# Kernel tuning notes

Hardware: AMD Instinct MI355X
Metric: run time of the kernel (lower is better)

Reference implementation:

```python
import jax, jax.numpy as jnp
import numpy as np

N_NODES = 100000
N_EDGES = 3200000
DIM = 64
N_LAYERS = 3


def setup_inputs() -> dict:
    key = jax.random.key(0)
    ks = jax.random.split(key, 8)
    x = jax.random.normal(ks[0], (N_NODES, DIM), dtype=jnp.float32)
    a = jax.random.uniform(ks[1], (N_EDGES,), dtype=jnp.float32)
    # weights stored as [in_dim, out_dim] so layer op is h @ W + b
    W1s = jax.random.normal(ks[2], (N_LAYERS, DIM, DIM), dtype=jnp.float32) * (1.0 / np.sqrt(DIM))
    b1s = jnp.zeros((N_LAYERS, DIM), dtype=jnp.float32)
    W2s = jax.random.normal(ks[3], (N_LAYERS, DIM, DIM), dtype=jnp.float32) * (1.0 / np.sqrt(DIM))
    b2s = jnp.zeros((N_LAYERS, DIM), dtype=jnp.float32)
    src = jax.random.randint(ks[4], (N_EDGES,), 0, N_NODES, dtype=jnp.int32)
    dst = jax.random.randint(ks[5], (N_EDGES,), 0, N_NODES, dtype=jnp.int32)
    return {"x": x, "a": a, "W1s": W1s, "b1s": b1s, "W2s": W2s, "b2s": b2s,
            "src": src, "dst": dst}


def reference(x, a, W1s, b1s, W2s, b2s, src, dst):
    """KGAT forward (eval mode, dropouts=0, normalize=False, full-graph blocks).

    Per layer: h_n[v] = sum_{e:(u->v)} a_e * h[u]
               h <- LeakyReLU((h + h_n) @ W1 + b1) + LeakyReLU((h * h_n) @ W2 + b2)
    Output: concat([x, h_1, h_2, h_3], axis=1) -> [N, 4*DIM]
    """
    n = x.shape[0]
    h = x
    embs = [x]
    for l in range(N_LAYERS):
        msg = h[src] * a[:, None]                      # [E, d] gather + edge scale
        h_n = jax.ops.segment_sum(msg, dst, num_segments=n)  # [N, d] scatter-add
        h = (jax.nn.leaky_relu((h + h_n) @ W1s[l] + b1s[l], 0.01)
             + jax.nn.leaky_relu((h * h_n) @ W2s[l] + b2s[l], 0.01))
        embs.append(h)
    return jnp.concatenate(embs, axis=1)
```

## Files before the change

kernel.cpp:

```cpp
#include <hip/hip_runtime.h>
#include <hip/hip_bf16.h>

#define N_NODES 100000
#define N_EDGES 3200000
#define DIM 64
#define OUT_COLS 256
#define BUCKET_SHIFT 8
#define NBUCK ((N_NODES + 255) / 256)
#define TILE 4096
#define NTILEBLK ((N_EDGES + TILE - 1) / TILE)
#define NODE_TILES ((N_NODES + 63) / 64)
#define WFRAG_PER_LAYER (2 * 2 * 4 * 64 * 8)

typedef __attribute__((ext_vector_type(8))) short short8;
typedef __attribute__((ext_vector_type(4))) float f32x4;

__device__ __forceinline__ unsigned short f2bf(float f) {
    __hip_bfloat16 b = __float2bfloat16(f);
    unsigned short u;
    __builtin_memcpy(&u, &b, 2);
    return u;
}
__device__ __forceinline__ unsigned int pkbf(float a, float b) {
    return (unsigned int)f2bf(a) | ((unsigned int)f2bf(b) << 16);
}
__device__ __forceinline__ float bflo(unsigned int p) { return __uint_as_float(p << 16); }
__device__ __forceinline__ float bfhi(unsigned int p) { return __uint_as_float(p & 0xFFFF0000u); }

__global__ void init_kernel(const float* __restrict__ x,
                            float* __restrict__ h,
                            unsigned short* __restrict__ h_bf,
                            float* __restrict__ out) {
    int i = blockIdx.x * blockDim.x + threadIdx.x;
    const int total = N_NODES * DIM / 4;
    if (i < total) {
        float4 v = ((const float4*)x)[i];
        ((float4*)h)[i] = v;
        int elem = i * 4;
        int node = elem >> 6;
        int c    = elem & 63;
        *(float4*)&out[node * OUT_COLS + c] = v;
        unsigned int lo = pkbf(v.x, v.y);
        unsigned int hi = pkbf(v.z, v.w);
        *(uint2*)&h_bf[elem] = make_uint2(lo, hi);
    }
}

__global__ __launch_bounds__(256) void wprep_kernel(const float* __restrict__ W1s,
                                                    const float* __restrict__ W2s,
                                                    unsigned short* __restrict__ wfrag) {
    int idx = blockIdx.x * 256 + threadIdx.x;
    if (idx >= 3 * WFRAG_PER_LAYER) return;
    int j     = idx & 7;
    int lane  = (idx >> 3) & 63;
    int ct    = (idx >> 9) & 3;
    int kt    = (idx >> 11) & 1;
    int mat   = (idx >> 12) & 1;
    int layer = idx >> 13;
    int k   = kt * 32 + (lane >> 4) * 8 + j;
    int col = ct * 16 + (lane & 15);
    const float* W = (mat ? W2s : W1s) + (size_t)layer * DIM * DIM;
    wfrag[idx] = f2bf(W[k * DIM + col]);
}

__global__ __launch_bounds__(256) void bucket_hist_kernel(const int* __restrict__ dst,
                                                          int* __restrict__ bucket_count) {
    __shared__ int lc[NBUCK];
    for (int b = threadIdx.x; b < NBUCK; b += 256) lc[b] = 0;
    __syncthreads();
    const int base = blockIdx.x * TILE;
#pragma unroll
    for (int k = 0; k < TILE / 256; ++k) {
        int e = base + k * 256 + threadIdx.x;
        if (e < N_EDGES) atomicAdd(&lc[((unsigned)dst[e]) >> BUCKET_SHIFT], 1);
    }
    __syncthreads();
    for (int b = threadIdx.x; b < NBUCK; b += 256) {
        int c = lc[b];
        if (c) atomicAdd(&bucket_count[b], c);
    }
}

__global__ __launch_bounds__(512) void bucket_scan_kernel(const int* __restrict__ bucket_count,
                                                          int* __restrict__ bucket_base,
                                                          int* __restrict__ bucket_cursor,
                                                          int* __restrict__ offsets) {
    __shared__ int s[512];
    const int t = threadIdx.x;
    int v = (t < NBUCK) ? bucket_count[t] : 0;
    s[t] = v;
    __syncthreads();
    for (int off = 1; off < 512; off <<= 1) {
        int u = (t >= off) ? s[t - off] : 0;
        __syncthreads();
        s[t] += u;
        __syncthreads();
    }
    if (t < NBUCK) { int b = s[t] - v; bucket_base[t] = b; bucket_cursor[t] = b; }
    if (t == 0) offsets[N_NODES] = N_EDGES;
}

__global__ __launch_bounds__(256) void binA_kernel(const int* __restrict__ src,
                                                   const int* __restrict__ dst,
                                                   const float* __restrict__ a,
                                                   int* __restrict__ bucket_cursor,
                                                   int2* __restrict__ temp) {
    __shared__ int lcount[NBUCK];
    __shared__ int lscan[512];
    __shared__ int lgbase[NBUCK];
    __shared__ int2 stage[TILE];
    __shared__ unsigned short sbuck[TILE];

    const int t = threadIdx.x;
    const int base = blockIdx.x * TILE;

    for (int b = t; b < NBUCK; b += 256) lcount[b] = 0;
    __syncthreads();

    int dv[TILE / 256], rk[TILE / 256];
#pragma unroll
    for (int k = 0; k < TILE / 256; ++k) {
        int e = base + k * 256 + t;
        dv[k] = 0; rk[k] = 0;
        if (e < N_EDGES) {
            int d = dst[e];
            dv[k] = d;
            rk[k] = atomicAdd(&lcount[((unsigned)d) >> BUCKET_SHIFT], 1);
        }
    }
    __syncthreads();

    lscan[t]       = (t < NBUCK) ? lcount[t] : 0;
    lscan[t + 256] = (t + 256 < NBUCK) ? lcount[t + 256] : 0;
    __syncthreads();
    for (int off = 1; off < 512; off <<= 1) {
        int u0 = (t >= off) ? lscan[t - off] : 0;
        int u1 = ((t + 256) >= off) ? lscan[t + 256 - off] : 0;
        __syncthreads();
        lscan[t] += u0;
        lscan[t + 256] += u1;
        __syncthreads();
    }
    for (int b = t; b < NBUCK; b += 256) {
        int c = lcount[b];
        int excl = lscan[b] - c;
        int g = 0;
        if (c) g = atomicAdd(&bucket_cursor[b], c);
        lgbase[b] = g - excl;
    }
    __syncthreads();

#pragma unroll
    for (int k = 0; k < TILE / 256; ++k) {
        int e = base + k * 256 + t;
        if (e < N_EDGES) {
            int d = dv[k];
            int b = ((unsigned)d) >> BUCKET_SHIFT;
            int slot = (lscan[b] - lcount[b]) + rk[k];
            stage[slot] = make_int2(src[e] | ((d & 255) << 24), __float_as_int(a[e]));
            sbuck[slot] = (unsigned short)b;
        }
    }
    __syncthreads();

    const int cntT = min(TILE, N_EDGES - base);
    for (int i = t; i < cntT; i += 256) {
        temp[lgbase[sbuck[i]] + i] = stage[i];
    }
}

__global__ __launch_bounds__(256) void binB_kernel(const int2* __restrict__ temp,
                                                   const int* __restrict__ bucket_base,
                                                   const int* __restrict__ bucket_count,
                                                   int* __restrict__ offsets,
                                                   int2* __restrict__ edges) {
    const int b = blockIdx.x;
    const int node0 = b << BUCKET_SHIFT;
    const int nodes = min(256, N_NODES - node0);
    const int beg = bucket_base[b];
    const int cnt = bucket_count[b];
    const int t = threadIdx.x;

    __shared__ int ncount[256];
    __shared__ int ssc[256];
    __shared__ int ncur[256];
    ncount[t] = 0;
    __syncthreads();
    for (int i = t; i < cnt; i += 256) {
        unsigned w0 = (unsigned)temp[beg + i].x;
        atomicAdd(&ncount[w0 >> 24], 1);
    }
    __syncthreads();
    int v = ncount[t];
    ssc[t] = v;
    __syncthreads();
    for (int off = 1; off < 256; off <<= 1) {
        int u = (t >= off) ? ssc[t - off] : 0;
        __syncthreads();
        ssc[t] += u;
        __syncthreads();
    }
    int excl = ssc[t] - v;
    if (t < nodes) offsets[node0 + t] = beg + excl;
    ncur[t] = beg + excl;
    __syncthreads();
    for (int i = t; i < cnt; i += 256) {
        int2 r = temp[beg + i];
        int loc = ((unsigned)r.x) >> 24;
        int pos = atomicAdd(&ncur[loc], 1);
        edges[pos] = make_int2(r.x & 0xFFFFFF, r.y);
    }
}

__global__ __launch_bounds__(256) void gather_kernel(
        const unsigned short* __restrict__ h_bf,
        const int2* __restrict__ edges,
        const int* __restrict__ offsets,
        float* __restrict__ hn) {
    const int lane   = threadIdx.x & 63;
    const int half   = lane >> 5;
    const int sub    = lane & 31;
    const int waveid = (blockIdx.x * blockDim.x + threadIdx.x) >> 6;
    const int node   = waveid * 2 + half;
    if (node >= N_NODES) return;

    const int beg = offsets[node];
    const int end = offsets[node + 1];
    const int col2 = sub * 2;

    float al0 = 0.f, al1 = 0.f, al2 = 0.f, al3 = 0.f;
    float ah0 = 0.f, ah1 = 0.f, ah2 = 0.f, ah3 = 0.f;
    int i = beg;
    for (; i + 4 <= end; i += 4) {
        int2 e0 = edges[i + 0];
        int2 e1 = edges[i + 1];
        int2 e2 = edges[i + 2];
        int2 e3 = edges[i + 3];
        unsigned int p0 = *(const unsigned int*)&h_bf[(size_t)e0.x * DIM + col2];
        unsigned int p1 = *(const unsigned int*)&h_bf[(size_t)e1.x * DIM + col2];
        unsigned int p2 = *(const unsigned int*)&h_bf[(size_t)e2.x * DIM + col2];
        unsigned int p3 = *(const unsigned int*)&h_bf[(size_t)e3.x * DIM + col2];
        float w0 = __int_as_float(e0.y);
        float w1 = __int_as_float(e1.y);
        float w2 = __int_as_float(e2.y);
        float w3 = __int_as_float(e3.y);
        al0 = fmaf(w0, bflo(p0), al0);  ah0 = fmaf(w0, bfhi(p0), ah0);
        al1 = fmaf(w1, bflo(p1), al1);  ah1 = fmaf(w1, bfhi(p1), ah1);
        al2 = fmaf(w2, bflo(p2), al2);  ah2 = fmaf(w2, bfhi(p2), ah2);
        al3 = fmaf(w3, bflo(p3), al3);  ah3 = fmaf(w3, bfhi(p3), ah3);
    }
    for (; i < end; ++i) {
        int2 e = edges[i];
        unsigned int p = *(const unsigned int*)&h_bf[(size_t)e.x * DIM + col2];
        float w = __int_as_float(e.y);
        al0 = fmaf(w, bflo(p), al0);
        ah0 = fmaf(w, bfhi(p), ah0);
    }
    float lo = (al0 + al1) + (al2 + al3);
    float hi = (ah0 + ah1) + (ah2 + ah3);
    *(float2*)&hn[(size_t)node * DIM + col2] = make_float2(lo, hi);
}

__global__ __launch_bounds__(256) void update_kernel(
        float* __restrict__ h,
        unsigned short* __restrict__ h_bf,
        const float* __restrict__ hn,
        const unsigned short* __restrict__ wfrag,
        const float* __restrict__ b1,
        const float* __restrict__ b2,
        float* __restrict__ out,
        int out_col_base) {
    __shared__ unsigned short t1s[64 * 64];
    __shared__ unsigned short t2s[64 * 64];

    const int t    = threadIdx.x;
    const int lane = t & 63;
    const int wid  = t >> 6;
    const int node0 = blockIdx.x * 64;

    short8 w1f[2][4], w2f[2][4];
#pragma unroll
    for (int kt = 0; kt < 2; ++kt)
#pragma unroll
        for (int ct = 0; ct < 4; ++ct) {
            w1f[kt][ct] = *(const short8*)(wfrag + (((0 * 2 + kt) * 4 + ct) * 64 + lane) * 8);
            w2f[kt][ct] = *(const short8*)(wfrag + (((1 * 2 + kt) * 4 + ct) * 64 + lane) * 8);
        }
    float bb1[4], bb2[4];
#pragma unroll
    for (int ct = 0; ct < 4; ++ct) {
        bb1[ct] = b1[ct * 16 + (lane & 15)];
        bb2[ct] = b2[ct * 16 + (lane & 15)];
    }

    {
        const int row = t >> 2;
        const int kc  = (t & 3) * 16;
        const int node = node0 + row;
        float tv1[16], tv2[16];
        if (node < N_NODES) {
            const float4* hp  = (const float4*)&h [(size_t)node * DIM + kc];
            const float4* hnp = (const float4*)&hn[(size_t)node * DIM + kc];
#pragma unroll
            for (int i = 0; i < 4; ++i) {
                float4 a = hp[i];
                float4 b = hnp[i];
                tv1[i * 4 + 0] = a.x + b.x;  tv2[i * 4 + 0] = a.x * b.x;
                tv1[i * 4 + 1] = a.y + b.y;  tv2[i * 4 + 1] = a.y * b.y;
                tv1[i * 4 + 2] = a.z + b.z;  tv2[i * 4 + 2] = a.z * b.z;
                tv1[i * 4 + 3] = a.w + b.w;  tv2[i * 4 + 3] = a.w * b.w;
            }
        } else {
#pragma unroll
            for (int i = 0; i < 16; ++i) { tv1[i] = 0.f; tv2[i] = 0.f; }
        }
        const int sw = (row & 7) << 4;
        const int base = row * 128 + (t & 3) * 32;
        uint4 q;
        q.x = pkbf(tv1[0], tv1[1]);  q.y = pkbf(tv1[2], tv1[3]);
        q.z = pkbf(tv1[4], tv1[5]);  q.w = pkbf(tv1[6], tv1[7]);
        *(uint4*)((char*)t1s + ((base) ^ sw)) = q;
        q.x = pkbf(tv1[8], tv1[9]);  q.y = pkbf(tv1[10], tv1[11]);
        q.z = pkbf(tv1[12], tv1[13]); q.w = pkbf(tv1[14], tv1[15]);
        *(uint4*)((char*)t1s + ((base + 16) ^ sw)) = q;
        q.x = pkbf(tv2[0], tv2[1]);  q.y = pkbf(tv2[2], tv2[3]);
        q.z = pkbf(tv2[4], tv2[5]);  q.w = pkbf(tv2[6], tv2[7]);
        *(uint4*)((char*)t2s + ((base) ^ sw)) = q;
        q.x = pkbf(tv2[8], tv2[9]);  q.y = pkbf(tv2[10], tv2[11]);
        q.z = pkbf(tv2[12], tv2[13]); q.w = pkbf(tv2[14], tv2[15]);
        *(uint4*)((char*)t2s + ((base + 16) ^ sw)) = q;
    }
    __syncthreads();

    const int arow = wid * 16 + (lane & 15);
    const int asw  = (arow & 7) << 4;
    short8 a1[2], a2[2];
#pragma unroll
    for (int kt = 0; kt < 2; ++kt) {
        int ab = (arow * 128 + kt * 64 + ((lane >> 4) << 4)) ^ asw;
        a1[kt] = *(const short8*)((const char*)t1s + ab);
        a2[kt] = *(const short8*)((const char*)t2s + ab);
    }

    f32x4 acc1[4], acc2[4];
#pragma unroll
    for (int ct = 0; ct < 4; ++ct) {
        acc1[ct] = (f32x4){bb1[ct], bb1[ct], bb1[ct], bb1[ct]};
        acc2[ct] = (f32x4){bb2[ct], bb2[ct], bb2[ct], bb2[ct]};
    }
#pragma unroll
    for (int ct = 0; ct < 4; ++ct) {
        acc1[ct] = __builtin_amdgcn_mfma_f32_16x16x32_bf16(a1[0], w1f[0][ct], acc1[ct], 0, 0, 0);
        acc1[ct] = __builtin_amdgcn_mfma_f32_16x16x32_bf16(a1[1], w1f[1][ct], acc1[ct], 0, 0, 0);
        acc2[ct] = __builtin_amdgcn_mfma_f32_16x16x32_bf16(a2[0], w2f[0][ct], acc2[ct], 0, 0, 0);
        acc2[ct] = __builtin_amdgcn_mfma_f32_16x16x32_bf16(a2[1], w2f[1][ct], acc2[ct], 0, 0, 0);
    }

#pragma unroll
    for (int ct = 0; ct < 4; ++ct) {
        const int col = ct * 16 + (lane & 15);
#pragma unroll
        for (int r = 0; r < 4; ++r) {
            const int grow = node0 + wid * 16 + (lane >> 4) * 4 + r;
            if (grow < N_NODES) {
                float v1 = acc1[ct][r]; v1 = v1 > 0.f ? v1 : 0.01f * v1;
                float v2 = acc2[ct][r]; v2 = v2 > 0.f ? v2 : 0.01f * v2;
                float hnew = v1 + v2;
                h[(size_t)grow * DIM + col] = hnew;
                h_bf[(size_t)grow * DIM + col] = f2bf(hnew);
                out[(size_t)grow * OUT_COLS + out_col_base + col] = hnew;
            }
        }
    }
}

extern "C" void kernel_launch(void* const* d_in, const int* in_sizes, int n_in,
                              void* d_out, int out_size, void* d_ws, size_t ws_size,
                              hipStream_t stream) {
    const float* x   = (const float*)d_in[0];
    const float* a   = (const float*)d_in[1];
    const float* W1s = (const float*)d_in[2];
    const float* b1s = (const float*)d_in[3];
    const float* W2s = (const float*)d_in[4];
    const float* b2s = (const float*)d_in[5];
    const int*   src = (const int*)d_in[6];
    const int*   dst = (const int*)d_in[7];
    float* out = (float*)d_out;

    float* h  = (float*)d_ws;
    float* hn = h + (size_t)N_NODES * DIM;
    unsigned short* h_bf = (unsigned short*)(hn + (size_t)N_NODES * DIM);
    int* offsets       = (int*)(h_bf + (size_t)N_NODES * DIM);
    int* bucket_count  = offsets + N_NODES + 1;
    int* bucket_base   = bucket_count + NBUCK;
    int* bucket_cursor = bucket_base + NBUCK;
    uintptr_t p = (uintptr_t)(bucket_cursor + NBUCK);
    p = (p + 15) & ~(uintptr_t)15;
    int2* edges = (int2*)p;
    int2* temp  = (int2*)hn;
    uintptr_t p2 = (uintptr_t)(edges + N_EDGES);
    p2 = (p2 + 15) & ~(uintptr_t)15;
    unsigned short* wfrag = (unsigned short*)p2;

    {
        int total = N_NODES * DIM / 4;
        init_kernel<<<(total + 255) / 256, 256, 0, stream>>>(x, h, h_bf, out);
    }

    wprep_kernel<<<(3 * WFRAG_PER_LAYER + 255) / 256, 256, 0, stream>>>(W1s, W2s, wfrag);

    hipMemsetAsync(bucket_count, 0, NBUCK * sizeof(int), stream);
    bucket_hist_kernel<<<NTILEBLK, 256, 0, stream>>>(dst, bucket_count);
    bucket_scan_kernel<<<1, 512, 0, stream>>>(bucket_count, bucket_base, bucket_cursor, offsets);
    binA_kernel<<<NTILEBLK, 256, 0, stream>>>(src, dst, a, bucket_cursor, temp);
    binB_kernel<<<NBUCK, 256, 0, stream>>>(temp, bucket_base, bucket_count, offsets, edges);

    for (int l = 0; l < 3; ++l) {
        int waves = (N_NODES + 1) / 2;
        int blocks = (waves * 64 + 255) / 256;
        gather_kernel<<<blocks, 256, 0, stream>>>(h_bf, edges, offsets, hn);
        update_kernel<<<NODE_TILES, 256, 0, stream>>>(
            h, h_bf, hn,
            wfrag + (size_t)l * WFRAG_PER_LAYER,
            b1s + (size_t)l * DIM,
            b2s + (size_t)l * DIM,
            out, (l + 1) * DIM);
    }
}
```

Measured before the change: 558.7 us.

## Replace global atomic bucket cursors with per-tile count matrix and column scan

The edge binning now writes per-tile bucket histograms to a matrix, and a new column-wise scan kernel turns that matrix into per-tile offsets. binA then computes its write positions deterministically instead of using global atomicAdd on bucket cursors, which also removes the memset. The aim is to avoid atomic contention and make the bucket layout stable, at the cost of an extra kernel launch and the matrix traffic (782x391 ints).

```diff
diff --git a/kernel.cpp b/kernel.cpp
--- a/kernel.cpp
+++ b/kernel.cpp
@@ -63,8 +63,8 @@
     wfrag[idx] = f2bf(W[k * DIM + col]);
 }
 
-__global__ __launch_bounds__(256) void bucket_hist_kernel(const int* __restrict__ dst,
-                                                          int* __restrict__ bucket_count) {
+__global__ __launch_bounds__(256) void count_kernel(const int* __restrict__ dst,
+                                                    int* __restrict__ mat) {
     __shared__ int lc[NBUCK];
     for (int b = threadIdx.x; b < NBUCK; b += 256) lc[b] = 0;
     __syncthreads();
@@ -75,15 +75,43 @@
         if (e < N_EDGES) atomicAdd(&lc[((unsigned)dst[e]) >> BUCKET_SHIFT], 1);
     }
     __syncthreads();
-    for (int b = threadIdx.x; b < NBUCK; b += 256) {
-        int c = lc[b];
-        if (c) atomicAdd(&bucket_count[b], c);
-    }
+    int* row = mat + (size_t)blockIdx.x * NBUCK;
+    for (int b = threadIdx.x; b < NBUCK; b += 256) row[b] = lc[b];
+}
+
+__global__ __launch_bounds__(256) void scan2_kernel(int* __restrict__ mat,
+                                                    int* __restrict__ bucket_count) {
+    const int b = blockIdx.x;
+    const int t = threadIdx.x;
+    int cpre[4];
+    int s = 0;
+#pragma unroll
+    for (int j = 0; j < 4; ++j) {
+        int blk = t * 4 + j;
+        cpre[j] = s;
+        int v = (blk < NTILEBLK) ? mat[(size_t)blk * NBUCK + b] : 0;
+        s += v;
+    }
+    __shared__ int ss[256];
+    ss[t] = s;
+    __syncthreads();
+    for (int off = 1; off < 256; off <<= 1) {
+        int u = (t >= off) ? ss[t - off] : 0;
+        __syncthreads();
+        ss[t] += u;
+        __syncthreads();
+    }
+    int excl = ss[t] - s;
+#pragma unroll
+    for (int j = 0; j < 4; ++j) {
+        int blk = t * 4 + j;
+        if (blk < NTILEBLK) mat[(size_t)blk * NBUCK + b] = excl + cpre[j];
+    }
+    if (t == 255) bucket_count[b] = ss[255];
 }
 
 __global__ __launch_bounds__(512) void bucket_scan_kernel(const int* __restrict__ bucket_count,
                                                           int* __restrict__ bucket_base,
-                                                          int* __restrict__ bucket_cursor,
                                                           int* __restrict__ offsets) {
     __shared__ int s[512];
     const int t = threadIdx.x;
@@ -96,14 +124,15 @@
         s[t] += u;
         __syncthreads();
     }
-    if (t < NBUCK) { int b = s[t] - v; bucket_base[t] = b; bucket_cursor[t] = b; }
+    if (t < NBUCK) bucket_base[t] = s[t] - v;
     if (t == 0) offsets[N_NODES] = N_EDGES;
 }
 
 __global__ __launch_bounds__(256) void binA_kernel(const int* __restrict__ src,
                                                    const int* __restrict__ dst,
                                                    const float* __restrict__ a,
-                                                   int* __restrict__ bucket_cursor,
+                                                   const int* __restrict__ bucket_base,
+                                                   const int* __restrict__ mat,
                                                    int2* __restrict__ temp) {
     __shared__ int lcount[NBUCK];
     __shared__ int lscan[512];
@@ -141,12 +170,12 @@
         lscan[t + 256] += u1;
         __syncthreads();
     }
-    for (int b = t; b < NBUCK; b += 256) {
-        int c = lcount[b];
-        int excl = lscan[b] - c;
-        int g = 0;
-        if (c) g = atomicAdd(&bucket_cursor[b], c);
-        lgbase[b] = g - excl;
+    {
+        const int* row = mat + (size_t)blockIdx.x * NBUCK;
+        for (int b = t; b < NBUCK; b += 256) {
+            int excl = lscan[b] - lcount[b];
+            lgbase[b] = bucket_base[b] + row[b] - excl;
+        }
     }
     __syncthreads();
 
@@ -393,14 +422,16 @@
     int* offsets       = (int*)(h_bf + (size_t)N_NODES * DIM);
     int* bucket_count  = offsets + N_NODES + 1;
     int* bucket_base   = bucket_count + NBUCK;
-    int* bucket_cursor = bucket_base + NBUCK;
-    uintptr_t p = (uintptr_t)(bucket_cursor + NBUCK);
+    uintptr_t p = (uintptr_t)(bucket_base + NBUCK);
     p = (p + 15) & ~(uintptr_t)15;
     int2* edges = (int2*)p;
     int2* temp  = (int2*)hn;
     uintptr_t p2 = (uintptr_t)(edges + N_EDGES);
     p2 = (p2 + 15) & ~(uintptr_t)15;
     unsigned short* wfrag = (unsigned short*)p2;
+    uintptr_t p3 = (uintptr_t)(wfrag + 3 * WFRAG_PER_LAYER);
+    p3 = (p3 + 15) & ~(uintptr_t)15;
+    int* mat = (int*)p3;
 
     {
         int total = N_NODES * DIM / 4;
@@ -409,10 +440,10 @@
 
     wprep_kernel<<<(3 * WFRAG_PER_LAYER + 255) / 256, 256, 0, stream>>>(W1s, W2s, wfrag);
 
-    hipMemsetAsync(bucket_count, 0, NBUCK * sizeof(int), stream);
-    bucket_hist_kernel<<<NTILEBLK, 256, 0, stream>>>(dst, bucket_count);
-    bucket_scan_kernel<<<1, 512, 0, stream>>>(bucket_count, bucket_base, bucket_cursor, offsets);
-    binA_kernel<<<NTILEBLK, 256, 0, stream>>>(src, dst, a, bucket_cursor, temp);
+    count_kernel<<<NTILEBLK, 256, 0, stream>>>(dst, mat);
+    scan2_kernel<<<NBUCK, 256, 0, stream>>>(mat, bucket_count);
+    bucket_scan_kernel<<<1, 512, 0, stream>>>(bucket_count, bucket_base, offsets);
+    binA_kernel<<<NTILEBLK, 256, 0, stream>>>(src, dst, a, bucket_base, mat, temp);
     binB_kernel<<<NBUCK, 256, 0, stream>>>(temp, bucket_base, bucket_count, offsets, edges);
 
     for (int l = 0; l < 3; ++l) {
```

Result: faster. 520.9 us (-6.8%).
